# Kernel tuning notes

Hardware: AMD Instinct MI355X
Metric: run time of the kernel (lower is better)

## Reference

```python
import jax, jax.numpy as jnp
import numpy as np
from jax import lax

B, T = 32, 768
N_MEL = 80
ENC_POS = 544  # encoder_output_dim(512) + positional_embedding_dim(32)
PRE = 256
RNN = 1024


def setup_inputs() -> dict:
    key = jax.random.key(0)
    ks = jax.random.split(key, 12)
    n = lambda k, shape, s: jax.random.normal(k, shape, jnp.float32) * s
    return {
        'duration_outputs': n(ks[0], (B, T, ENC_POS), 1.0),
        'decoder_inputs': n(ks[1], (B, N_MEL, T), 1.0),
        'memory_lengths': jax.random.randint(ks[2], (B,), 1, T + 1, dtype=jnp.int32),
        'pre_w1': n(ks[3], (N_MEL, PRE), 0.05),
        'pre_w2': n(ks[4], (PRE, PRE), 0.05),
        'rnn1_wx': n(ks[5], (PRE + ENC_POS, 4 * RNN), 0.02),
        'rnn1_wh': n(ks[6], (RNN, 4 * RNN), 0.02),
        'rnn1_b': jnp.zeros(4 * RNN, jnp.float32),
        'rnn1_g': jnp.ones(4 * RNN, jnp.float32),
        'rnn1_bn': jnp.zeros(4 * RNN, jnp.float32),
        'rnn1_gc': jnp.ones(RNN, jnp.float32),
        'rnn1_bc': jnp.zeros(RNN, jnp.float32),
        'rnn2_wx': n(ks[7], (RNN, 4 * RNN), 0.02),
        'rnn2_wh': n(ks[8], (RNN, 4 * RNN), 0.02),
        'rnn2_b': jnp.zeros(4 * RNN, jnp.float32),
        'rnn2_g': jnp.ones(4 * RNN, jnp.float32),
        'rnn2_bn': jnp.zeros(4 * RNN, jnp.float32),
        'rnn2_gc': jnp.ones(RNN, jnp.float32),
        'rnn2_bc': jnp.zeros(RNN, jnp.float32),
        'proj_w': n(ks[9], (RNN + ENC_POS, N_MEL), 0.02),
        'proj_b': jnp.zeros(N_MEL, jnp.float32),
    }


def _ln(x, g, b):
    m = jnp.mean(x, axis=-1, keepdims=True)
    v = jnp.var(x, axis=-1, keepdims=True)
    return (x - m) * lax.rsqrt(v + 1e-5) * g + b


def _lstm_norm_cell(x, h, c, wx, wh, b, g, bn, gc, bc):
    # layer-normalized LSTM cell: LN over gate pre-activations + LN on cell
    z = _ln(x @ wx + h @ wh + b, g, bn)            # [B, 4H]
    i, f, gg, o = jnp.split(z, 4, axis=-1)
    c = jax.nn.sigmoid(f) * c + jax.nn.sigmoid(i) * jnp.tanh(gg)
    h = jax.nn.sigmoid(o) * jnp.tanh(_ln(c, gc, bc))
    return h, c


def reference(duration_outputs, decoder_inputs, memory_lengths,
              pre_w1, pre_w2,
              rnn1_wx, rnn1_wh, rnn1_b, rnn1_g, rnn1_bn, rnn1_gc, rnn1_bc,
              rnn2_wx, rnn2_wh, rnn2_b, rnn2_g, rnn2_bn, rnn2_gc, rnn2_bc,
              proj_w, proj_b):
    b = decoder_inputs.shape[0]
    t = decoder_inputs.shape[2]
    # parse_decoder_inputs: [B, M, T] -> [T, B, M]; prepend go frame
    dec = jnp.transpose(decoder_inputs, (2, 0, 1))
    dec = jnp.concatenate([jnp.zeros((1, b, N_MEL), dec.dtype), dec], axis=0)  # [T+1,B,M]
    # prenet (dropout disabled for deterministic reference)
    x = jax.nn.relu(dec @ pre_w1)
    x = jax.nn.relu(x @ pre_w2)
    pre = x[:t]                                            # [T, B, PRE]
    dur = jnp.transpose(duration_outputs, (1, 0, 2))       # [T, B, ENC_POS]

    def step(carry, xs):
        h1, c1, h2, c2 = carry
        p, d = xs
        cell_in = jnp.concatenate([p, d], axis=-1)
        h1, c1 = _lstm_norm_cell(cell_in, h1, c1, rnn1_wx, rnn1_wh, rnn1_b, rnn1_g, rnn1_bn, rnn1_gc, rnn1_bc)
        h2, c2 = _lstm_norm_cell(h1, h2, c2, rnn2_wx, rnn2_wh, rnn2_b, rnn2_g, rnn2_bn, rnn2_gc, rnn2_bc)
        out = jnp.concatenate([h2, d], axis=-1) @ proj_w + proj_b  # [B, M]
        return (h1, c1, h2, c2), out

    init = tuple(jnp.zeros((b, RNN), jnp.float32) for _ in range(4))
    _, mel = lax.scan(step, init, (pre, dur))              # [T, B, M]
    return jnp.transpose(mel, (1, 2, 0))                   # [B, M, T]
```

## Files before the change

### kernel.cpp

```cpp
#include <hip/hip_runtime.h>
#include <cstdint>
#include <cstddef>

typedef _Float16 f16;
typedef _Float16 f16x8 __attribute__((ext_vector_type(8)));
typedef float f32x4 __attribute__((ext_vector_type(4)));

#define MFMA_F16(a,b,c) __builtin_amdgcn_mfma_f32_16x16x32_f16((a),(b),(c),0,0,0)

#define NCLS 16
#define CT_A1 0
#define CT_H1 1
#define CT_A2 2
#define CT_H2 3
#define CT_C  4

__device__ __forceinline__ float sigf(float x){ return 1.f/(1.f + expf(-x)); }

__device__ __forceinline__ void st_wt_f32(float* p, float v){
  asm volatile("global_store_dword %0, %1, off sc0 sc1" :: "v"(p), "v"(v) : "memory");
}
__device__ __forceinline__ void st_wt_u32(f16* p, unsigned v){
  asm volatile("global_store_dword %0, %1, off sc0 sc1" :: "v"(p), "v"(v) : "memory");
}
__device__ __forceinline__ void vm_drain(){ asm volatile("s_waitcnt vmcnt(0)" ::: "memory"); }

template<int N> __device__ __forceinline__ void vm_waitN(){
  asm volatile("s_waitcnt vmcnt(%0)" :: "i"(N) : "memory");
  __builtin_amdgcn_sched_barrier(0);
}

__device__ __forceinline__ void bar_arrive(unsigned* c){
  __hip_atomic_fetch_add(c, 1u, __ATOMIC_RELAXED, __HIP_MEMORY_SCOPE_AGENT);
}
__device__ __forceinline__ void spin_ge(const unsigned* p, unsigned target){
  while (__hip_atomic_load(p, __ATOMIC_RELAXED, __HIP_MEMORY_SCOPE_AGENT) < target)
    __builtin_amdgcn_s_sleep(1);
}

__device__ __forceinline__ void ld_8f32(const float* p, f32x4& a, f32x4& b){
  asm volatile(
    "global_load_dwordx4 %0, %2, off sc0 sc1\n\t"
    "global_load_dwordx4 %1, %2, off offset:16 sc0 sc1\n\t"
    "s_waitcnt vmcnt(0)"
    : "=&v"(a), "=&v"(b) : "v"(p) : "memory");
}

__device__ __forceinline__ void ld8_issue(const f16* p, f16x8* f){
  asm volatile(
    "global_load_dwordx4 %0, %8, off sc0 sc1\n\t"
    "global_load_dwordx4 %1, %8, off offset:64 sc0 sc1\n\t"
    "global_load_dwordx4 %2, %8, off offset:128 sc0 sc1\n\t"
    "global_load_dwordx4 %3, %8, off offset:192 sc0 sc1\n\t"
    "global_load_dwordx4 %4, %8, off offset:256 sc0 sc1\n\t"
    "global_load_dwordx4 %5, %8, off offset:320 sc0 sc1\n\t"
    "global_load_dwordx4 %6, %8, off offset:384 sc0 sc1\n\t"
    "global_load_dwordx4 %7, %8, off offset:448 sc0 sc1"
    : "=&v"(f[0]),"=&v"(f[1]),"=&v"(f[2]),"=&v"(f[3]),
      "=&v"(f[4]),"=&v"(f[5]),"=&v"(f[6]),"=&v"(f[7])
    : "v"(p) : "memory");
}

__device__ __forceinline__ f32x4 gemm32r(const f16* hp, const f16x8* bfrag){
  f32x4 a = {0.f,0.f,0.f,0.f};
  f16x8 fA[8], fB[8];
  ld8_issue(hp,       fA);
  ld8_issue(hp + 256, fB);
  vm_waitN<8>();
  #pragma unroll
  for (int kk = 0; kk < 8; ++kk) a = MFMA_F16(fA[kk], bfrag[kk], a);
  ld8_issue(hp + 512, fA);
  vm_waitN<8>();
  #pragma unroll
  for (int kk = 0; kk < 8; ++kk) a = MFMA_F16(fB[kk], bfrag[8 + kk], a);
  ld8_issue(hp + 768, fB);
  vm_waitN<8>();
  #pragma unroll
  for (int kk = 0; kk < 8; ++kk) a = MFMA_F16(fA[kk], bfrag[16 + kk], a);
  vm_waitN<0>();
  #pragma unroll
  for (int kk = 0; kk < 8; ++kk) a = MFMA_F16(fB[kk], bfrag[24 + kk], a);
  return a;
}

__global__ __launch_bounds__(256) void k_transpose_f16(const float* __restrict__ src,
    f16* __restrict__ dst, int K, int N, int dstStride, int dstOff){
  const int n0 = blockIdx.x*32, k0 = blockIdx.y*32, tid = threadIdx.x;
  __shared__ float tl[32][33];
  #pragma unroll
  for (int rep = 0; rep < 4; ++rep){
    int e = rep*256 + tid; int i = e >> 5, j = e & 31;
    int k = k0 + i, n = n0 + j;
    tl[i][j] = (k < K && n < N) ? src[(size_t)k*N + n] : 0.f;
  }
  __syncthreads();
  #pragma unroll
  for (int rep = 0; rep < 4; ++rep){
    int e = rep*256 + tid; int i2 = e & 31, j2 = e >> 5;
    int n = n0 + j2, k = k0 + i2;
    if (k < K && n < N) dst[(size_t)n*dstStride + dstOff + k] = (f16)tl[i2][j2];
  }
}

__global__ __launch_bounds__(256) void k_prenet(const float* __restrict__ dec,
    const float* __restrict__ w1, const float* __restrict__ w2, f16* __restrict__ cellin){
  const int t = blockIdx.x, tid = threadIdx.x;
  __shared__ float sin_[32][81];
  __shared__ f16   w1T[256][88];
  __shared__ float x1s[32][260];
  __shared__ f16   w2c[256][72];
  __shared__ f16   xo[32][256];
  for (int e = tid; e < 32*80; e += 256){
    int i = e/80, m = e - i*80;
    sin_[i][m] = (t == 0) ? 0.f : dec[(size_t)i*61440 + (size_t)m*768 + (t-1)];
  }
  for (int e = tid; e < 80*256; e += 256){ int m = e >> 8, j = e & 255; w1T[j][m] = (f16)w1[e]; }
  __syncthreads();
  const int j = tid;
  for (int i = 0; i < 32; ++i){
    float a = 0.f;
    #pragma unroll
    for (int m8 = 0; m8 < 10; ++m8){
      f16x8 wvv = *(const f16x8*)&w1T[j][m8*8];
      #pragma unroll
      for (int l = 0; l < 8; ++l) a += (float)wvv[l] * sin_[i][m8*8 + l];
    }
    x1s[i][j] = fmaxf(a, 0.f);
  }
  __syncthreads();
  float acc2[32];
  #pragma unroll
  for (int i = 0; i < 32; ++i) acc2[i] = 0.f;
  for (int c = 0; c < 4; ++c){
    for (int e = tid; e < 64*256; e += 256){
      int kl = e >> 8, jj = e & 255;
      w2c[jj][kl] = (f16)w2[(size_t)(c*64 + kl)*256 + jj];
    }
    __syncthreads();
    f16x8 wv8[8];
    #pragma unroll
    for (int k8 = 0; k8 < 8; ++k8) wv8[k8] = *(const f16x8*)&w2c[j][k8*8];
    for (int i = 0; i < 32; ++i){
      float a = 0.f;
      #pragma unroll
      for (int k8 = 0; k8 < 8; ++k8)
        #pragma unroll
        for (int l = 0; l < 8; ++l) a += (float)wv8[k8][l]*x1s[i][c*64 + k8*8 + l];
      acc2[i] += a;
    }
    __syncthreads();
  }
  for (int i = 0; i < 32; ++i) xo[i][j] = (f16)fmaxf(acc2[i], 0.f);
  __syncthreads();
  for (int e = tid; e < 32*256; e += 256){
    int i = e >> 8, jj = e & 255;
    cellin[((size_t)t*32 + i)*800 + jj] = xo[i][jj];
  }
}

__global__ __launch_bounds__(256) void k_durfill(const float* __restrict__ dur, f16* __restrict__ cellin){
  const int t = blockIdx.x, tid = threadIdx.x;
  for (int e = tid; e < 32*544; e += 256){
    int b = e / 544, c = e - b*544;
    cellin[((size_t)t*32 + b)*800 + 256 + c] = (f16)dur[(size_t)b*417792 + (size_t)t*544 + c];
  }
}

__global__ __launch_bounds__(256) void k_ws_report(float* __restrict__ out, int n, float val){
  int i = blockIdx.x*256 + threadIdx.x;
  if (i < n) out[i] = val;
}

__global__ __launch_bounds__(512, 1) void k_recurrence(
    const f16* __restrict__ cellin, const f16* __restrict__ wxT1,
    const f16* __restrict__ whT1, const f16* __restrict__ w2T,
    f16* __restrict__ H2all, f16* __restrict__ h1buf, f16* __restrict__ h2buf,
    float* __restrict__ zbuf1, float* __restrict__ zbuf2,
    unsigned* __restrict__ ctrs,
    const float* __restrict__ b1v,
    const float* __restrict__ g1, const float* __restrict__ bn1,
    const float* __restrict__ gc1v, const float* __restrict__ bc1v,
    const float* __restrict__ b2v,
    const float* __restrict__ g2, const float* __restrict__ bn2,
    const float* __restrict__ gc2v, const float* __restrict__ bc2v)
{
  const int tid = threadIdx.x, blk = blockIdx.x;
  const int lane = tid & 63, wv = tid >> 6;
  const int r16 = lane & 15, quad = lane >> 4;
  const int part = wv >> 2, pair = wv & 3, rt = pair >> 1, ct = pair & 1;
  const int g_b = ct*2 + (r16 >> 3), u_b = r16 & 7;
  const int zrow = tid >> 4, zc0 = tid & 15, zc1 = (tid & 15) + 16;
  const int zrt = zrow >> 4, zi = zrow & 15;
  const int arow = rt*16 + r16;

  __shared__ f16   swx[3200*8];
  __shared__ float zredA[8][16][17];
  __shared__ float zredX[2][4][16][17];
  __shared__ float zs[4096];
  __shared__ float wredS1[8], wredQ1[8], wredS2[8], wredQ2[8];

  f16x8 bfrag[32];

  if (blk < 128){
    const int cls = blk & 15, ub0 = blk*8;
    const int colg = (g_b << 10) + ub0 + u_b;
    if (part == 0){
      #pragma unroll
      for (int c = 0; c < 32; ++c)
        bfrag[c] = *(const f16x8*)(whT1 + (size_t)colg*1024 + c*32 + quad*8);
    }
    for (int idx = tid; idx < 3200; idx += 512){
      int l = idx & 15, q = (idx >> 4) & 3, v = idx >> 6;
      int c = v % 25, ctx = v / 25;
      int gg = ctx*2 + (l >> 3), uu = l & 7;
      int cg = (gg << 10) + ub0 + uu;
      *(f16x8*)(swx + idx*8) = *(const f16x8*)(wxT1 + (size_t)cg*800 + c*32 + q*8);
    }
    const float zb0 = b1v[((zc0 >> 3) << 10) + ub0 + (zc0 & 7)];
    const float zb1 = b1v[((zc1 >> 3) << 10) + ub0 + (zc1 & 7)];
    float pgv[4][2], pbv[4][2], gcv[2], bcv[2], cst[2] = {0.f, 0.f};
    if (blk < 32){
      #pragma unroll
      for (int k = 0; k < 2; ++k){
        const int u = 2*tid + k;
        #pragma unroll
        for (int g = 0; g < 4; ++g){
          pgv[g][k] = g1[(g << 10) + u]; pbv[g][k] = bn1[(g << 10) + u];
        }
        gcv[k] = gc1v[u]; bcv[k] = bc1v[u];
      }
    }
    __syncthreads();
    if (part == 1){
      f32x4 a = {0.f,0.f,0.f,0.f};
      const f16* ap = cellin + (size_t)arow*800 + quad*8;
      for (int c = 0; c < 25; ++c){
        f16x8 av = *(const f16x8*)(ap + c*32);
        f16x8 bx = *(const f16x8*)(swx + (size_t)(((ct*25 + c)*4 + quad)*16 + r16)*8);
        a = MFMA_F16(av, bx, a);
      }
      #pragma unroll
      for (int reg = 0; reg < 4; ++reg) zredX[0][wv-4][quad*4 + reg][r16] = a[reg];
    }
    for (int t = 0; t < 768; ++t){
      if (t > 0 && tid < 16) spin_ge(ctrs + (CT_H1*NCLS + tid)*16, 2u*t);
      __syncthreads();
      if (part == 0){
        if (t > 0){
          const f16* hp = h1buf + (size_t)((t+1)&1)*32768 + (size_t)arow*1024 + quad*8;
          f32x4 a = gemm32r(hp, bfrag);
          #pragma unroll
          for (int reg = 0; reg < 4; ++reg) zredA[wv][quad*4 + reg][r16] = a[reg];
        } else {
          #pragma unroll
          for (int reg = 0; reg < 4; ++reg) zredA[wv][quad*4 + reg][r16] = 0.f;
        }
      } else if (t < 767){
        f32x4 a = {0.f,0.f,0.f,0.f};
        const f16* ap = cellin + (size_t)(t+1)*25600 + (size_t)arow*800 + quad*8;
        for (int c = 0; c < 25; ++c){
          f16x8 av = *(const f16x8*)(ap + c*32);
          f16x8 bx = *(const f16x8*)(swx + (size_t)(((ct*25 + c)*4 + quad)*16 + r16)*8);
          a = MFMA_F16(av, bx, a);
        }
        #pragma unroll
        for (int reg = 0; reg < 4; ++reg) zredX[(t+1)&1][wv-4][quad*4 + reg][r16] = a[reg];
      }
      __syncthreads();
      {
        const int xs = t & 1;
        float za  = zredA[zrt*2    ][zi][zc0] + zredX[xs][zrt*2    ][zi][zc0] + zb0;
        float zbv = zredA[zrt*2 + 1][zi][zc0] + zredX[xs][zrt*2 + 1][zi][zc0] + zb1;
        float* zp = zbuf1 + (size_t)zrow*4096;
        st_wt_f32(zp + ((zc0 >> 3) << 10) + ub0 + (zc0 & 7), za);
        st_wt_f32(zp + ((zc1 >> 3) << 10) + ub0 + (zc1 & 7), zbv);
      }
      vm_drain(); __syncthreads();
      if (tid == 0) bar_arrive(ctrs + (CT_A1*NCLS + cls)*16);
      if (blk < 32){
        if (tid < 16) spin_ge(ctrs + (CT_A1*NCLS + tid)*16, 8u*(t+1));
        else if (t >= 2 && tid < 32) spin_ge(ctrs + (CT_C*NCLS + (tid-16))*16, 8u*(t-1));
        __syncthreads();
        f32x4 va, vb;
        ld_8f32(zbuf1 + (size_t)blk*4096 + tid*8, va, vb);
        *(f32x4*)(zs + tid*8)     = va;
        *(f32x4*)(zs + tid*8 + 4) = vb;
        float s = va.x+va.y+va.z+va.w + vb.x+vb.y+vb.z+vb.w;
        float q = va.x*va.x+va.y*va.y+va.z*va.z+va.w*va.w
                + vb.x*vb.x+vb.y*vb.y+vb.z*vb.z+vb.w*vb.w;
        s += __shfl_down(s, 32); q += __shfl_down(q, 32);
        s += __shfl_down(s, 16); q += __shfl_down(q, 16);
        s += __shfl_down(s, 8);  q += __shfl_down(q, 8);
        s += __shfl_down(s, 4);  q += __shfl_down(q, 4);
        s += __shfl_down(s, 2);  q += __shfl_down(q, 2);
        s += __shfl_down(s, 1);  q += __shfl_down(q, 1);
        if (lane == 0){ wredS1[wv] = s; wredQ1[wv] = q; }
        __syncthreads();
        float S = 0.f, Q = 0.f;
        #pragma unroll
        for (int w = 0; w < 8; ++w){ S += wredS1[w]; Q += wredQ1[w]; }
        const float m1 = S * (1.f/4096.f);
        const float rs1 = rsqrtf(Q*(1.f/4096.f) - m1*m1 + 1e-5f);
        float oo[2];
        #pragma unroll
        for (int k = 0; k < 2; ++k){
          const int u = 2*tid + k;
          const float ziv = (zs[u]        - m1)*rs1*pgv[0][k] + pbv[0][k];
          const float zf  = (zs[1024 + u] - m1)*rs1*pgv[1][k] + pbv[1][k];
          const float zg  = (zs[2048 + u] - m1)*rs1*pgv[2][k] + pbv[2][k];
          const float zo  = (zs[3072 + u] - m1)*rs1*pgv[3][k] + pbv[3][k];
          cst[k] = sigf(zf)*cst[k] + sigf(ziv)*tanhf(zg);
          oo[k] = sigf(zo);
        }
        float s2 = cst[0] + cst[1], q2 = cst[0]*cst[0] + cst[1]*cst[1];
        s2 += __shfl_down(s2, 32); q2 += __shfl_down(q2, 32);
        s2 += __shfl_down(s2, 16); q2 += __shfl_down(q2, 16);
        s2 += __shfl_down(s2, 8);  q2 += __shfl_down(q2, 8);
        s2 += __shfl_down(s2, 4);  q2 += __shfl_down(q2, 4);
        s2 += __shfl_down(s2, 2);  q2 += __shfl_down(q2, 2);
        s2 += __shfl_down(s2, 1);  q2 += __shfl_down(q2, 1);
        if (lane == 0){ wredS2[wv] = s2; wredQ2[wv] = q2; }
        __syncthreads();
        float S2 = 0.f, Q2 = 0.f;
        #pragma unroll
        for (int w = 0; w < 8; ++w){ S2 += wredS2[w]; Q2 += wredQ2[w]; }
        const float m2 = S2 * (1.f/1024.f);
        const float rs2 = rsqrtf(Q2*(1.f/1024.f) - m2*m2 + 1e-5f);
        union { f16 f[2]; unsigned u32v; } pk;
        #pragma unroll
        for (int k = 0; k < 2; ++k){
          float arg = fmaf(fmaf(cst[k], rs2, -m2*rs2), gcv[k], bcv[k]);
          float e = exp2f(arg * 2.885390081777927f);
          pk.f[k] = (f16)(oo[k] * fmaf(-2.f, __builtin_amdgcn_rcpf(e + 1.f), 1.f));
        }
        st_wt_u32(h1buf + (size_t)(t&1)*32768 + blk*1024 + 2*tid, pk.u32v);
        vm_drain(); __syncthreads();
        if (tid == 0) bar_arrive(ctrs + (CT_H1*NCLS + (blk & 15))*16);
      }
    }
  } else {
    const int blk2 = blk - 128, cls = blk2 & 15, ub0 = blk2*8;
    const int colg = (g_b << 10) + ub0 + u_b;
    {
      const f16* wsrc = w2T + (size_t)colg*2048 + (part == 0 ? 1024 : 0);
      #pragma unroll
      for (int c = 0; c < 32; ++c)
        bfrag[c] = *(const f16x8*)(wsrc + c*32 + quad*8);
    }
    const float zb0 = b2v[((zc0 >> 3) << 10) + ub0 + (zc0 & 7)];
    const float zb1 = b2v[((zc1 >> 3) << 10) + ub0 + (zc1 & 7)];
    float pgv[4][2], pbv[4][2], gcv[2], bcv[2], cst[2] = {0.f, 0.f};
    if (blk2 < 32){
      #pragma unroll
      for (int k = 0; k < 2; ++k){
        const int u = 2*tid + k;
        #pragma unroll
        for (int g = 0; g < 4; ++g){
          pgv[g][k] = g2[(g << 10) + u]; pbv[g][k] = bn2[(g << 10) + u];
        }
        gcv[k] = gc2v[u]; bcv[k] = bc2v[u];
      }
    }
    __syncthreads();
    for (int t = 0; t < 768; ++t){
      if (tid < 16) spin_ge(ctrs + (CT_H1*NCLS + tid)*16, 2u*(t+1));
      else if (t > 0 && tid < 32) spin_ge(ctrs + (CT_H2*NCLS + (tid-16))*16, 2u*t);
      __syncthreads();
      if (part == 0 && t == 0){
        #pragma unroll
        for (int reg = 0; reg < 4; ++reg) zredA[wv][quad*4 + reg][r16] = 0.f;
      } else {
        const f16* hp = (part == 0)
          ? h2buf + (size_t)((t+1)&1)*32768 + (size_t)arow*1024 + quad*8
          : h1buf + (size_t)(t&1)*32768     + (size_t)arow*1024 + quad*8;
        f32x4 a = gemm32r(hp, bfrag);
        #pragma unroll
        for (int reg = 0; reg < 4; ++reg) zredA[wv][quad*4 + reg][r16] = a[reg];
      }
      __syncthreads();
      if (tid == 64) bar_arrive(ctrs + (CT_C*NCLS + cls)*16);
      {
        float za  = zredA[zrt*2    ][zi][zc0] + zredA[4 + zrt*2    ][zi][zc0] + zb0;
        float zbv = zredA[zrt*2 + 1][zi][zc0] + zredA[4 + zrt*2 + 1][zi][zc0] + zb1;
        float* zp = zbuf2 + (size_t)zrow*4096;
        st_wt_f32(zp + ((zc0 >> 3) << 10) + ub0 + (zc0 & 7), za);
        st_wt_f32(zp + ((zc1 >> 3) << 10) + ub0 + (zc1 & 7), zbv);
      }
      vm_drain(); __syncthreads();
      if (tid == 0) bar_arrive(ctrs + (CT_A2*NCLS + cls)*16);
      if (blk2 < 32){
        if (tid < 16) spin_ge(ctrs + (CT_A2*NCLS + tid)*16, 8u*(t+1));
        __syncthreads();
        f32x4 va, vb;
        ld_8f32(zbuf2 + (size_t)blk2*4096 + tid*8, va, vb);
        *(f32x4*)(zs + tid*8)     = va;
        *(f32x4*)(zs + tid*8 + 4) = vb;
        float s = va.x+va.y+va.z+va.w + vb.x+vb.y+vb.z+vb.w;
        float q = va.x*va.x+va.y*va.y+va.z*va.z+va.w*va.w
                + vb.x*vb.x+vb.y*vb.y+vb.z*vb.z+vb.w*vb.w;
        s += __shfl_down(s, 32); q += __shfl_down(q, 32);
        s += __shfl_down(s, 16); q += __shfl_down(q, 16);
        s += __shfl_down(s, 8);  q += __shfl_down(q, 8);
        s += __shfl_down(s, 4);  q += __shfl_down(q, 4);
        s += __shfl_down(s, 2);  q += __shfl_down(q, 2);
        s += __shfl_down(s, 1);  q += __shfl_down(q, 1);
        if (lane == 0){ wredS1[wv] = s; wredQ1[wv] = q; }
        __syncthreads();
        float S = 0.f, Q = 0.f;
        #pragma unroll
        for (int w = 0; w < 8; ++w){ S += wredS1[w]; Q += wredQ1[w]; }
        const float m1 = S * (1.f/4096.f);
        const float rs1 = rsqrtf(Q*(1.f/4096.f) - m1*m1 + 1e-5f);
        float oo[2];
        #pragma unroll
        for (int k = 0; k < 2; ++k){
          const int u = 2*tid + k;
          const float ziv = (zs[u]        - m1)*rs1*pgv[0][k] + pbv[0][k];
          const float zf  = (zs[1024 + u] - m1)*rs1*pgv[1][k] + pbv[1][k];
          const float zg  = (zs[2048 + u] - m1)*rs1*pgv[2][k] + pbv[2][k];
          const float zo  = (zs[3072 + u] - m1)*rs1*pgv[3][k] + pbv[3][k];
          cst[k] = sigf(zf)*cst[k] + sigf(ziv)*tanhf(zg);
          oo[k] = sigf(zo);
        }
        float s2 = cst[0] + cst[1], q2 = cst[0]*cst[0] + cst[1]*cst[1];
        s2 += __shfl_down(s2, 32); q2 += __shfl_down(q2, 32);
        s2 += __shfl_down(s2, 16); q2 += __shfl_down(q2, 16);
        s2 += __shfl_down(s2, 8);  q2 += __shfl_down(q2, 8);
        s2 += __shfl_down(s2, 4);  q2 += __shfl_down(q2, 4);
        s2 += __shfl_down(s2, 2);  q2 += __shfl_down(q2, 2);
        s2 += __shfl_down(s2, 1);  q2 += __shfl_down(q2, 1);
        if (lane == 0){ wredS2[wv] = s2; wredQ2[wv] = q2; }
        __syncthreads();
        float S2 = 0.f, Q2 = 0.f;
        #pragma unroll
        for (int w = 0; w < 8; ++w){ S2 += wredS2[w]; Q2 += wredQ2[w]; }
        const float m2 = S2 * (1.f/1024.f);
        const float rs2 = rsqrtf(Q2*(1.f/1024.f) - m2*m2 + 1e-5f);
        union { f16 f[2]; unsigned u32v; } pk;
        #pragma unroll
        for (int k = 0; k < 2; ++k){
          float arg = fmaf(fmaf(cst[k], rs2, -m2*rs2), gcv[k], bcv[k]);
          float e = exp2f(arg * 2.885390081777927f);
          pk.f[k] = (f16)(oo[k] * fmaf(-2.f, __builtin_amdgcn_rcpf(e + 1.f), 1.f));
        }
        st_wt_u32(h2buf + (size_t)(t&1)*32768 + blk2*1024 + 2*tid, pk.u32v);
        st_wt_u32(H2all + (size_t)(t+1)*32768 + blk2*1024 + 2*tid, pk.u32v);
        vm_drain(); __syncthreads();
        if (tid == 0) bar_arrive(ctrs + (CT_H2*NCLS + (blk2 & 15))*16);
      }
    }
  }
}

__global__ __launch_bounds__(256) void k_proj(const f16* __restrict__ H2all, const f16* __restrict__ cellin,
    const f16* __restrict__ projT, const float* __restrict__ projb, float* __restrict__ out){
  const int t = blockIdx.x, tid = threadIdx.x;
  const int lane = tid & 63, wv = tid >> 6;
  const int r16 = lane & 15, quad = lane >> 4;
  __shared__ float pred[4][32][84];
  f32x4 acc[2][5] = {};
  const f16* H2 = H2all + (size_t)(t+1)*32768;
  const f16* CI = cellin + (size_t)t*32*800;
  const int kbeg = wv*13;
  const int kend = (wv == 3) ? 49 : (kbeg + 13);
  for (int ks = kbeg; ks < kend; ++ks){
    const int k0 = ks*32 + quad*8;
    f16x8 a0, a1;
    if (ks < 32){
      a0 = *(const f16x8*)(H2 + r16*1024 + k0);
      a1 = *(const f16x8*)(H2 + (16+r16)*1024 + k0);
    } else {
      a0 = *(const f16x8*)(CI + r16*800 + 256 + (k0 - 1024));
      a1 = *(const f16x8*)(CI + (16+r16)*800 + 256 + (k0 - 1024));
    }
    f16x8 bf[5];
    #pragma unroll
    for (int nt = 0; nt < 5; ++nt)
      bf[nt] = *(const f16x8*)(projT + (size_t)(nt*16 + r16)*1568 + k0);
    #pragma unroll
    for (int nt = 0; nt < 5; ++nt){
      acc[0][nt] = MFMA_F16(a0, bf[nt], acc[0][nt]);
      acc[1][nt] = MFMA_F16(a1, bf[nt], acc[1][nt]);
    }
  }
  #pragma unroll
  for (int mt = 0; mt < 2; ++mt)
    #pragma unroll
    for (int nt = 0; nt < 5; ++nt)
      #pragma unroll
      for (int reg = 0; reg < 4; ++reg)
        pred[wv][mt*16 + quad*4 + reg][nt*16 + r16] = acc[mt][nt][reg];
  __syncthreads();
  for (int e = tid; e < 2560; e += 256){
    int m = e >> 5, b = e & 31;
    float v = pred[0][b][m] + pred[1][b][m] + pred[2][b][m] + pred[3][b][m] + projb[m];
    out[(size_t)b*61440 + (size_t)m*768 + t] = v;
  }
}

extern "C" void kernel_launch(void* const* d_in, const int* in_sizes, int n_in,
                              void* d_out, int out_size, void* d_ws, size_t ws_size,
                              hipStream_t stream)
{
  const float* duration = (const float*)d_in[0];
  const float* decoder  = (const float*)d_in[1];
  const float* pre_w1   = (const float*)d_in[3];
  const float* pre_w2   = (const float*)d_in[4];
  const float* rnn1_wx  = (const float*)d_in[5];
  const float* rnn1_wh  = (const float*)d_in[6];
  const float* rnn1_b   = (const float*)d_in[7];
  const float* rnn1_g   = (const float*)d_in[8];
  const float* rnn1_bn  = (const float*)d_in[9];
  const float* rnn1_gc  = (const float*)d_in[10];
  const float* rnn1_bc  = (const float*)d_in[11];
  const float* rnn2_wx  = (const float*)d_in[12];
  const float* rnn2_wh  = (const float*)d_in[13];
  const float* rnn2_b   = (const float*)d_in[14];
  const float* rnn2_g   = (const float*)d_in[15];
  const float* rnn2_bn  = (const float*)d_in[16];
  const float* rnn2_gc  = (const float*)d_in[17];
  const float* rnn2_bc  = (const float*)d_in[18];
  const float* proj_w   = (const float*)d_in[19];
  const float* proj_b   = (const float*)d_in[20];
  float* out = (float*)d_out;

  char* w = (char*)d_ws;
  f16* cellin = (f16*)w;      w += (size_t)24576*800*2;
  f16* wxT1   = (f16*)w;      w += (size_t)4096*800*2;
  f16* whT1   = (f16*)w;      w += (size_t)4096*1024*2;
  f16* w2T    = (f16*)w;      w += (size_t)4096*2048*2;
  f16* projT  = (f16*)w;      w += 262144;
  f16* H2all  = (f16*)w;      w += (size_t)769*32768*2;
  f16* h1buf  = (f16*)w;      w += 131072;
  f16* h2buf  = (f16*)w;      w += 131072;
  float* zbuf1 = (float*)w;   w += (size_t)32*4096*4;
  float* zbuf2 = (float*)w;   w += (size_t)32*4096*4;
  unsigned* ctrs = (unsigned*)w; w += 8192;
  const size_t need = (size_t)((char*)w - (char*)d_ws);
  if (ws_size < need){
    k_ws_report<<<(out_size + 255)/256, 256, 0, stream>>>(out, out_size, (float)(ws_size >> 20));
    return;
  }

  (void)hipMemsetAsync(ctrs, 0, 8192, stream);
  (void)hipMemsetAsync(h1buf, 0, 131072, stream);
  (void)hipMemsetAsync(h2buf, 0, 131072, stream);

  k_transpose_f16<<<dim3(4096/32, 25), 256, 0, stream>>>(rnn1_wx, wxT1, 800, 4096, 800, 0);
  k_transpose_f16<<<dim3(4096/32, 32), 256, 0, stream>>>(rnn1_wh, whT1, 1024, 4096, 1024, 0);
  k_transpose_f16<<<dim3(4096/32, 32), 256, 0, stream>>>(rnn2_wx, w2T, 1024, 4096, 2048, 0);
  k_transpose_f16<<<dim3(4096/32, 32), 256, 0, stream>>>(rnn2_wh, w2T, 1024, 4096, 2048, 1024);
  k_transpose_f16<<<dim3(3, 49), 256, 0, stream>>>(proj_w, projT, 1568, 80, 1568, 0);
  k_prenet<<<768, 256, 0, stream>>>(decoder, pre_w1, pre_w2, cellin);
  k_durfill<<<768, 256, 0, stream>>>(duration, cellin);
  k_recurrence<<<256, 512, 0, stream>>>(cellin, wxT1, whT1, w2T, H2all, h1buf, h2buf,
      zbuf1, zbuf2, ctrs,
      rnn1_b, rnn1_g, rnn1_bn, rnn1_gc, rnn1_bc,
      rnn2_b, rnn2_g, rnn2_bn, rnn2_gc, rnn2_bc);
  k_proj<<<768, 256, 0, stream>>>(H2all, cellin, projT, proj_b, out);
}
```

Baseline: 10.91 ms.

## Replace atomic counter barriers with per-block tag flags and deepen h1 buffering

Swaps the atomic fetch-add counters used for inter-block synchronisation in the persistent recurrence kernel for per-block monotonic tags written with plain write-through stores and polled with uncached loads, spreading waits across more threads. The h1 ring buffer grows from two to four slots so layer 1 can run further ahead of layer 2 (the cell-stage wait slack goes from two to four steps). It also replaces tanhf and expf-based sigmoid with exp2/rcp fast approximations. This removes atomic contention on shared counters but relies on store and load visibility ordering without atomics, and the fast math slightly changes numerics.

```diff
diff --git a/kernel.cpp b/kernel.cpp
--- a/kernel.cpp
+++ b/kernel.cpp
@@ -8,34 +8,40 @@
 
 #define MFMA_F16(a,b,c) __builtin_amdgcn_mfma_f32_16x16x32_f16((a),(b),(c),0,0,0)
 
-#define NCLS 16
-#define CT_A1 0
-#define CT_H1 1
-#define CT_A2 2
-#define CT_H2 3
-#define CT_C  4
-
-__device__ __forceinline__ float sigf(float x){ return 1.f/(1.f + expf(-x)); }
+#define LOG2E  1.4426950408889634f
+#define LOG2E2 2.885390081777927f
+
+__device__ __forceinline__ float sigf(float x){
+  return __builtin_amdgcn_rcpf(1.f + exp2f(-x * LOG2E));
+}
+__device__ __forceinline__ float tanhfast(float x){
+  float e = exp2f(x * LOG2E2);
+  return fmaf(-2.f, __builtin_amdgcn_rcpf(e + 1.f), 1.f);
+}
 
 __device__ __forceinline__ void st_wt_f32(float* p, float v){
   asm volatile("global_store_dword %0, %1, off sc0 sc1" :: "v"(p), "v"(v) : "memory");
 }
 __device__ __forceinline__ void st_wt_u32(f16* p, unsigned v){
   asm volatile("global_store_dword %0, %1, off sc0 sc1" :: "v"(p), "v"(v) : "memory");
+}
+__device__ __forceinline__ void st_tag(unsigned* p, unsigned v){
+  asm volatile("global_store_dword %0, %1, off sc0 sc1" :: "v"(p), "v"(v) : "memory");
+}
+__device__ __forceinline__ void tag_wait(const unsigned* p, unsigned target){
+  for (;;){
+    unsigned v;
+    asm volatile("global_load_dword %0, %1, off sc0 sc1\n\ts_waitcnt vmcnt(0)"
+                 : "=v"(v) : "v"(p) : "memory");
+    if (v >= target) return;
+    __builtin_amdgcn_s_sleep(1);
+  }
 }
 __device__ __forceinline__ void vm_drain(){ asm volatile("s_waitcnt vmcnt(0)" ::: "memory"); }
 
 template<int N> __device__ __forceinline__ void vm_waitN(){
   asm volatile("s_waitcnt vmcnt(%0)" :: "i"(N) : "memory");
   __builtin_amdgcn_sched_barrier(0);
-}
-
-__device__ __forceinline__ void bar_arrive(unsigned* c){
-  __hip_atomic_fetch_add(c, 1u, __ATOMIC_RELAXED, __HIP_MEMORY_SCOPE_AGENT);
-}
-__device__ __forceinline__ void spin_ge(const unsigned* p, unsigned target){
-  while (__hip_atomic_load(p, __ATOMIC_RELAXED, __HIP_MEMORY_SCOPE_AGENT) < target)
-    __builtin_amdgcn_s_sleep(1);
 }
 
 __device__ __forceinline__ void ld_8f32(const float* p, f32x4& a, f32x4& b){
@@ -176,7 +182,7 @@
     const f16* __restrict__ whT1, const f16* __restrict__ w2T,
     f16* __restrict__ H2all, f16* __restrict__ h1buf, f16* __restrict__ h2buf,
     float* __restrict__ zbuf1, float* __restrict__ zbuf2,
-    unsigned* __restrict__ ctrs,
+    unsigned* __restrict__ tags,
     const float* __restrict__ b1v,
     const float* __restrict__ g1, const float* __restrict__ bn1,
     const float* __restrict__ gc1v, const float* __restrict__ bc1v,
@@ -193,6 +199,12 @@
   const int zrt = zrow >> 4, zi = zrow & 15;
   const int arow = rt*16 + r16;
 
+  unsigned* ztag1 = tags;
+  unsigned* ztag2 = tags + 2048;
+  unsigned* htag1 = tags + 4096;
+  unsigned* htag2 = tags + 4608;
+  unsigned* ctag  = tags + 5120;
+
   __shared__ f16   swx[3200*8];
   __shared__ float zredA[8][16][17];
   __shared__ float zredX[2][4][16][17];
@@ -202,7 +214,7 @@
   f16x8 bfrag[32];
 
   if (blk < 128){
-    const int cls = blk & 15, ub0 = blk*8;
+    const int ub0 = blk*8;
     const int colg = (g_b << 10) + ub0 + u_b;
     if (part == 0){
       #pragma unroll
@@ -243,11 +255,11 @@
       for (int reg = 0; reg < 4; ++reg) zredX[0][wv-4][quad*4 + reg][r16] = a[reg];
     }
     for (int t = 0; t < 768; ++t){
-      if (t > 0 && tid < 16) spin_ge(ctrs + (CT_H1*NCLS + tid)*16, 2u*t);
+      if (t > 0 && tid < 32) tag_wait(htag1 + tid*16, (unsigned)t);
       __syncthreads();
       if (part == 0){
         if (t > 0){
-          const f16* hp = h1buf + (size_t)((t+1)&1)*32768 + (size_t)arow*1024 + quad*8;
+          const f16* hp = h1buf + (size_t)((t-1)&3)*32768 + (size_t)arow*1024 + quad*8;
           f32x4 a = gemm32r(hp, bfrag);
           #pragma unroll
           for (int reg = 0; reg < 4; ++reg) zredA[wv][quad*4 + reg][r16] = a[reg];
@@ -276,10 +288,10 @@
         st_wt_f32(zp + ((zc1 >> 3) << 10) + ub0 + (zc1 & 7), zbv);
       }
       vm_drain(); __syncthreads();
-      if (tid == 0) bar_arrive(ctrs + (CT_A1*NCLS + cls)*16);
+      if (tid == 0) st_tag(ztag1 + blk*16, (unsigned)(t+1));
       if (blk < 32){
-        if (tid < 16) spin_ge(ctrs + (CT_A1*NCLS + tid)*16, 8u*(t+1));
-        else if (t >= 2 && tid < 32) spin_ge(ctrs + (CT_C*NCLS + (tid-16))*16, 8u*(t-1));
+        if (tid < 128) tag_wait(ztag1 + tid*16, (unsigned)(t+1));
+        else if (t >= 4 && tid < 256) tag_wait(ctag + (tid-128)*16, (unsigned)(t-3));
         __syncthreads();
         f32x4 va, vb;
         ld_8f32(zbuf1 + (size_t)blk*4096 + tid*8, va, vb);
@@ -309,7 +321,7 @@
           const float zf  = (zs[1024 + u] - m1)*rs1*pgv[1][k] + pbv[1][k];
           const float zg  = (zs[2048 + u] - m1)*rs1*pgv[2][k] + pbv[2][k];
           const float zo  = (zs[3072 + u] - m1)*rs1*pgv[3][k] + pbv[3][k];
-          cst[k] = sigf(zf)*cst[k] + sigf(ziv)*tanhf(zg);
+          cst[k] = sigf(zf)*cst[k] + sigf(ziv)*tanhfast(zg);
           oo[k] = sigf(zo);
         }
         float s2 = cst[0] + cst[1], q2 = cst[0]*cst[0] + cst[1]*cst[1];
@@ -330,16 +342,16 @@
         #pragma unroll
         for (int k = 0; k < 2; ++k){
           float arg = fmaf(fmaf(cst[k], rs2, -m2*rs2), gcv[k], bcv[k]);
-          float e = exp2f(arg * 2.885390081777927f);
+          float e = exp2f(arg * LOG2E2);
           pk.f[k] = (f16)(oo[k] * fmaf(-2.f, __builtin_amdgcn_rcpf(e + 1.f), 1.f));
         }
-        st_wt_u32(h1buf + (size_t)(t&1)*32768 + blk*1024 + 2*tid, pk.u32v);
+        st_wt_u32(h1buf + (size_t)(t&3)*32768 + blk*1024 + 2*tid, pk.u32v);
         vm_drain(); __syncthreads();
-        if (tid == 0) bar_arrive(ctrs + (CT_H1*NCLS + (blk & 15))*16);
+        if (tid == 0) st_tag(htag1 + blk*16, (unsigned)(t+1));
       }
     }
   } else {
-    const int blk2 = blk - 128, cls = blk2 & 15, ub0 = blk2*8;
+    const int blk2 = blk - 128, ub0 = blk2*8;
     const int colg = (g_b << 10) + ub0 + u_b;
     {
       const f16* wsrc = w2T + (size_t)colg*2048 + (part == 0 ? 1024 : 0);
@@ -363,8 +375,8 @@
     }
     __syncthreads();
     for (int t = 0; t < 768; ++t){
-      if (tid < 16) spin_ge(ctrs + (CT_H1*NCLS + tid)*16, 2u*(t+1));
-      else if (t > 0 && tid < 32) spin_ge(ctrs + (CT_H2*NCLS + (tid-16))*16, 2u*t);
+      if (tid < 32) tag_wait(htag1 + tid*16, (unsigned)(t+1));
+      else if (t > 0 && tid < 64) tag_wait(htag2 + (tid-32)*16, (unsigned)t);
       __syncthreads();
       if (part == 0 && t == 0){
         #pragma unroll
@@ -372,13 +384,13 @@
       } else {
         const f16* hp = (part == 0)
           ? h2buf + (size_t)((t+1)&1)*32768 + (size_t)arow*1024 + quad*8
-          : h1buf + (size_t)(t&1)*32768     + (size_t)arow*1024 + quad*8;
+          : h1buf + (size_t)(t&3)*32768     + (size_t)arow*1024 + quad*8;
         f32x4 a = gemm32r(hp, bfrag);
         #pragma unroll
         for (int reg = 0; reg < 4; ++reg) zredA[wv][quad*4 + reg][r16] = a[reg];
       }
       __syncthreads();
-      if (tid == 64) bar_arrive(ctrs + (CT_C*NCLS + cls)*16);
+      if (tid == 0) st_tag(ctag + blk2*16, (unsigned)(t+1));
       {
         float za  = zredA[zrt*2    ][zi][zc0] + zredA[4 + zrt*2    ][zi][zc0] + zb0;
         float zbv = zredA[zrt*2 + 1][zi][zc0] + zredA[4 + zrt*2 + 1][zi][zc0] + zb1;
@@ -387,9 +399,9 @@
         st_wt_f32(zp + ((zc1 >> 3) << 10) + ub0 + (zc1 & 7), zbv);
       }
       vm_drain(); __syncthreads();
-      if (tid == 0) bar_arrive(ctrs + (CT_A2*NCLS + cls)*16);
+      if (tid == 0) st_tag(ztag2 + blk2*16, (unsigned)(t+1));
       if (blk2 < 32){
-        if (tid < 16) spin_ge(ctrs + (CT_A2*NCLS + tid)*16, 8u*(t+1));
+        if (tid < 128) tag_wait(ztag2 + tid*16, (unsigned)(t+1));
         __syncthreads();
         f32x4 va, vb;
         ld_8f32(zbuf2 + (size_t)blk2*4096 + tid*8, va, vb);
@@ -419,7 +431,7 @@
           const float zf  = (zs[1024 + u] - m1)*rs1*pgv[1][k] + pbv[1][k];
           const float zg  = (zs[2048 + u] - m1)*rs1*pgv[2][k] + pbv[2][k];
           const float zo  = (zs[3072 + u] - m1)*rs1*pgv[3][k] + pbv[3][k];
-          cst[k] = sigf(zf)*cst[k] + sigf(ziv)*tanhf(zg);
+          cst[k] = sigf(zf)*cst[k] + sigf(ziv)*tanhfast(zg);
           oo[k] = sigf(zo);
         }
         float s2 = cst[0] + cst[1], q2 = cst[0]*cst[0] + cst[1]*cst[1];
@@ -440,13 +452,13 @@
         #pragma unroll
         for (int k = 0; k < 2; ++k){
           float arg = fmaf(fmaf(cst[k], rs2, -m2*rs2), gcv[k], bcv[k]);
-          float e = exp2f(arg * 2.885390081777927f);
+          float e = exp2f(arg * LOG2E2);
           pk.f[k] = (f16)(oo[k] * fmaf(-2.f, __builtin_amdgcn_rcpf(e + 1.f), 1.f));
         }
         st_wt_u32(h2buf + (size_t)(t&1)*32768 + blk2*1024 + 2*tid, pk.u32v);
         st_wt_u32(H2all + (size_t)(t+1)*32768 + blk2*1024 + 2*tid, pk.u32v);
         vm_drain(); __syncthreads();
-        if (tid == 0) bar_arrive(ctrs + (CT_H2*NCLS + (blk2 & 15))*16);
+        if (tid == 0) st_tag(htag2 + blk2*16, (unsigned)(t+1));
       }
     }
   }
@@ -531,19 +543,19 @@
   f16* w2T    = (f16*)w;      w += (size_t)4096*2048*2;
   f16* projT  = (f16*)w;      w += 262144;
   f16* H2all  = (f16*)w;      w += (size_t)769*32768*2;
-  f16* h1buf  = (f16*)w;      w += 131072;
+  f16* h1buf  = (f16*)w;      w += 262144;
   f16* h2buf  = (f16*)w;      w += 131072;
   float* zbuf1 = (float*)w;   w += (size_t)32*4096*4;
   float* zbuf2 = (float*)w;   w += (size_t)32*4096*4;
-  unsigned* ctrs = (unsigned*)w; w += 8192;
+  unsigned* tags = (unsigned*)w; w += 28672;
   const size_t need = (size_t)((char*)w - (char*)d_ws);
   if (ws_size < need){
     k_ws_report<<<(out_size + 255)/256, 256, 0, stream>>>(out, out_size, (float)(ws_size >> 20));
     return;
   }
 
-  (void)hipMemsetAsync(ctrs, 0, 8192, stream);
-  (void)hipMemsetAsync(h1buf, 0, 131072, stream);
+  (void)hipMemsetAsync(tags, 0, 28672, stream);
+  (void)hipMemsetAsync(h1buf, 0, 262144, stream);
   (void)hipMemsetAsync(h2buf, 0, 131072, stream);
 
   k_transpose_f16<<<dim3(4096/32, 25), 256, 0, stream>>>(rnn1_wx, wxT1, 800, 4096, 800, 0);
@@ -554,7 +566,7 @@
   k_prenet<<<768, 256, 0, stream>>>(decoder, pre_w1, pre_w2, cellin);
   k_durfill<<<768, 256, 0, stream>>>(duration, cellin);
   k_recurrence<<<256, 512, 0, stream>>>(cellin, wxT1, whT1, w2T, H2all, h1buf, h2buf,
-      zbuf1, zbuf2, ctrs,
+      zbuf1, zbuf2, tags,
       rnn1_b, rnn1_g, rnn1_bn, rnn1_gc, rnn1_bc,
       rnn2_b, rnn2_g, rnn2_bn, rnn2_gc, rnn2_bc);
   k_proj<<<768, 256, 0, stream>>>(H2all, cellin, projT, proj_b, out);
```

After: 10.22 ms. 6.3% less time.
